# Kernel optimization log

Hardware: AMD Instinct MI355X
Metric: run time of the kernel (lower is better)

The kernel has to match this reference:

```python
import jax, jax.numpy as jnp
import numpy as np
from jax import lax

HEADS = 4
DIM_HEAD = 64


def setup_inputs() -> dict:
    key = jax.random.key(0)
    k1, k2, k3 = jax.random.split(key, 3)
    B, C, H, W = 4, 256, 64, 64
    x = jax.random.normal(k1, (B, C, H, W), dtype=jnp.float32)
    # depthwise 3x3 conv weight, groups=C -> OIHW with O=C, I=1
    w_dw = jax.random.normal(k2, (C, 1, 3, 3), dtype=jnp.float32) * 0.1
    # pointwise 1x1 conv weight C -> 3C (stored as [out, in])
    w_pw = jax.random.normal(k3, (3 * C, C), dtype=jnp.float32) * 0.05
    return {"x": x, "w_dw": w_dw, "w_pw": w_pw}


def reference(x, w_dw, w_pw):
    B, C, H, W = x.shape
    S = H * W
    scale = DIM_HEAD ** -0.5
    # depthwise separable conv QKV projection (no bias)
    dw = lax.conv_general_dilated(
        x, w_dw, window_strides=(1, 1), padding=((1, 1), (1, 1)),
        feature_group_count=C, dimension_numbers=("NCHW", "OIHW", "NCHW"))
    qkv = jnp.einsum("bchw,oc->bohw", dw, w_pw)  # [B, 3C, H, W]
    q, k, v = jnp.split(qkv, 3, axis=1)

    def to_heads(t):
        # b (h d) ih iw -> b h (ih iw) d
        t = t.reshape(B, HEADS, DIM_HEAD, S)
        return jnp.transpose(t, (0, 1, 3, 2))  # [B, h, S, d]

    q, k, v = to_heads(q), to_heads(k), to_heads(v)
    dots = jnp.einsum("bhsd,bhtd->bhst", q, k) * scale  # [B, h, S, S]
    attn = jax.nn.softmax(dots, axis=-1)
    out = jnp.einsum("bhst,bhtd->bhsd", attn, v)  # [B, h, S, d]
    # b h (ih iw) d -> b (h d) ih iw
    out = jnp.transpose(out, (0, 1, 3, 2)).reshape(B, C, H, W)
    return out
```

## Files before the change

### kernel.cpp

```cpp
#include <hip/hip_runtime.h>


typedef __attribute__((ext_vector_type(8))) __bf16 bf16x8;
typedef __attribute__((ext_vector_type(4))) float f32x4;
typedef __attribute__((ext_vector_type(16))) float f32x16;
typedef __attribute__((ext_vector_type(8))) unsigned short ushort8;
typedef __attribute__((ext_vector_type(4))) unsigned int uint4v;

#define OFF_DW 0ull
#define OFF_WB 8388608ull
#define OFF_Q  8781824ull
#define OFF_K  17170432ull
#define OFF_V  25559040ull

__device__ __forceinline__ unsigned short f2bf(float x) {
  unsigned u = __builtin_bit_cast(unsigned, x);
  u += 0x7fffu + ((u >> 16) & 1u);
  return (unsigned short)(u >> 16);
}

__device__ __forceinline__ void gld16(const void* g, void* l) {
  __builtin_amdgcn_global_load_lds((const __attribute__((address_space(1))) void*)g,
                                   (__attribute__((address_space(3))) void*)l, 16, 0, 0);
}

__device__ __forceinline__ unsigned cvtpk(float lo, float hi) {
  unsigned r;
  asm("v_cvt_pk_bf16_f32 %0, %1, %2" : "=v"(r) : "v"(lo), "v"(hi));
  return r;
}

__global__ __launch_bounds__(256) void k_wcvt(const float* __restrict__ wpw,
                                              unsigned short* __restrict__ wbf) {
  int idx = blockIdx.x * 256 + threadIdx.x;
  int o = idx >> 8;
  float v = wpw[idx];
  if (o < 256) v *= 0.18033688011112042f;
  wbf[idx] = f2bf(v);
}

__global__ __launch_bounds__(256) void k_dw(const float* __restrict__ x,
                                            const float* __restrict__ wdw,
                                            unsigned short* __restrict__ dwt) {
  __shared__ float tile[64 * 65];
  const int t = threadIdx.x;
  const int h = blockIdx.x;
  const int c0 = blockIdx.y * 64;
  const int b = blockIdx.z;
  const int w = t & 63;
  const int wq = t >> 6;
#pragma unroll
  for (int i = 0; i < 16; ++i) {
    int cl = wq * 16 + i;
    int c = c0 + cl;
    const float* wd = wdw + c * 9;
    const float* xb = x + ((size_t)(b * 256 + c) * 64) * 64;
    float acc = 0.f;
#pragma unroll
    for (int ky = 0; ky < 3; ++ky) {
      int hh = h + ky - 1;
      if ((unsigned)hh < 64u) {
        const float* row = xb + hh * 64;
#pragma unroll
        for (int kx = 0; kx < 3; ++kx) {
          int ww = w + kx - 1;
          if ((unsigned)ww < 64u) acc += row[ww] * wd[ky * 3 + kx];
        }
      }
    }
    tile[w * 65 + cl] = acc;
  }
  __syncthreads();
  int sl = t >> 2, cch = (t & 3) * 16;
  ushort8 p0, p1;
#pragma unroll
  for (int j = 0; j < 8; ++j) p0[j] = f2bf(tile[sl * 65 + cch + j]);
#pragma unroll
  for (int j = 0; j < 8; ++j) p1[j] = f2bf(tile[sl * 65 + cch + 8 + j]);
  unsigned short* dst = dwt + ((size_t)(b * 4096 + h * 64 + sl)) * 256 + c0 + cch;
  *(ushort8*)dst = p0;
  *(ushort8*)(dst + 8) = p1;
}

__global__ __launch_bounds__(512) void k_pw(const unsigned short* __restrict__ dwt,
                                            const unsigned short* __restrict__ wbf,
                                            unsigned short* __restrict__ q,
                                            unsigned short* __restrict__ k,
                                            unsigned short* __restrict__ v) {
  __shared__ __align__(16) unsigned char smem[114944];
  const int t = threadIdx.x;
  const int lane = t & 63, wv = t >> 6;
  const int s0 = blockIdx.x * 64;
  const int b = blockIdx.y;
  const int vb = ((lane >> 5) << 9) + (((lane & 31) ^ (lane >> 5)) << 4);
  const char* dsrc = (const char*)dwt + ((size_t)(b * 4096 + s0)) * 512;
#pragma unroll
  for (int i = 0; i < 4; ++i) {
    int I = wv * 4 + i;
    int u = ((2 * i) & 7) << 4;
    gld16(dsrc + (size_t)I * 1024 + (vb ^ u), smem + 65536 + I * 1024);
    gld16((const char*)wbf + (size_t)I * 1024 + (vb ^ u), smem + I * 1024);
  }
  asm volatile("s_waitcnt vmcnt(0)" ::: "memory");
  __syncthreads();

  const int c15 = lane & 15, g = lane >> 4;
  const int wo = wv >> 1, ws = wv & 1;
  const int orow = wo * 16 + c15;

#pragma unroll 1
  for (int yy = 0; yy < 12; ++yy) {
    const unsigned char* wbuf = smem + (yy & 1) * 32768;
    if (yy < 11) {
      unsigned char* wnext = smem + ((yy + 1) & 1) * 32768;
#pragma unroll
      for (int i = 0; i < 4; ++i) {
        int I = wv * 4 + i;
        int u = ((2 * i) & 7) << 4;
        gld16((const char*)wbf + (size_t)(yy + 1) * 32768 + (size_t)I * 1024 + (vb ^ u),
              wnext + I * 1024);
      }
    }

    f32x4 acc[2] = {{0,0,0,0},{0,0,0,0}};
#pragma unroll
    for (int kc = 0; kc < 8; ++kc) {
      bf16x8 a = *(const bf16x8*)(wbuf + orow * 512 + (((kc * 4 + g) ^ (orow & 7)) << 4));
#pragma unroll
      for (int nt = 0; nt < 2; ++nt) {
        int srow = (ws * 2 + nt) * 16 + c15;
        bf16x8 bb = *(const bf16x8*)(smem + 65536 + srow * 512 + (((kc * 4 + g) ^ (srow & 7)) << 4));
        acc[nt] = __builtin_amdgcn_mfma_f32_16x16x32_bf16(a, bb, acc[nt], 0, 0, 0);
      }
    }

    const int type = yy >> 2, head = yy & 3;
    const size_t bh = (size_t)(b * 4 + head);
    if (type == 2) {
#pragma unroll
      for (int nt = 0; nt < 2; ++nt)
#pragma unroll
        for (int r = 0; r < 4; ++r) {
          int d = wo * 16 + g * 4 + r;
          int sg = s0 + (ws * 2 + nt) * 16 + c15;
          v[(bh * 64 + d) * 4096 + sg] = f2bf(acc[nt][r]);
        }
    } else {
      float* ol = (float*)(smem + 98304);
#pragma unroll
      for (int nt = 0; nt < 2; ++nt)
#pragma unroll
        for (int r = 0; r < 4; ++r)
          ol[((ws * 2 + nt) * 16 + c15) * 65 + (wo * 16 + g * 4 + r)] = acc[nt][r];
      __syncthreads();
      unsigned short* dst0 = (type == 0) ? q : k;
      int sl = t >> 3, dch = (t & 7) * 8;
      ushort8 p0;
#pragma unroll
      for (int j = 0; j < 8; ++j) p0[j] = f2bf(ol[sl * 65 + dch + j]);
      unsigned short* dst = dst0 + (bh * 4096 + s0 + sl) * 64 + dch;
      *(ushort8*)dst = p0;
    }

    asm volatile("s_waitcnt vmcnt(0)" ::: "memory");
    __syncthreads();
  }
}

__global__ __launch_bounds__(512) void k_attn(const unsigned short* __restrict__ qg,
                                              const unsigned short* __restrict__ kg,
                                              const unsigned short* __restrict__ vg,
                                              float* __restrict__ out) {
  __shared__ __align__(16) unsigned char smem[98304];
  const int t = threadIdx.x;
  const int lane = t & 63, wv = t >> 6;
  const int l31 = lane & 31, hi = lane >> 5;

  const int blk = blockIdx.x;
  const int xcd = blk & 7, idx = blk >> 3;
  const int bh = xcd * 2 + (idx & 1);
  const int s0 = (idx >> 1) * 256;

  const char* qsrc = (const char*)qg + (size_t)bh * 524288 + (size_t)s0 * 128;
  const char* ksrc = (const char*)kg + (size_t)bh * 524288;
  const char* vsrc = (const char*)vg + (size_t)bh * 524288;
  const int vQK = ((lane >> 3) << 7) + (((lane & 7) ^ (lane >> 3)) << 4);
  const int vV  = ((lane >> 3) << 13) + (((lane & 7) ^ (lane >> 3)) << 4);
  int kpoff[2];
  {
#pragma unroll
    for (int i = 0; i < 2; ++i) {
      int I = (wv & 3) * 2 + i;
      int srb = I * 8 + (lane >> 3);
      if (((srb >> 2) + 1) & 2) srb ^= 12;
      kpoff[i] = srb * 128 + (((lane & 7) ^ (lane >> 3)) << 4);
    }
  }

#pragma unroll
  for (int i = 0; i < 4; ++i) {
    int I = wv * 4 + i;
    gld16(qsrc + (size_t)I * 1024 + vQK, smem + I * 1024);
  }
#pragma unroll
  for (int tt = 0; tt < 2; ++tt) {
    unsigned char* tb = smem + 32768 + tt * 16384;
    if (wv < 4) {
#pragma unroll
      for (int i = 0; i < 2; ++i) {
        int I = wv * 2 + i;
        gld16(ksrc + (size_t)tt * 8192 + kpoff[i], tb + I * 1024);
      }
    } else {
#pragma unroll
      for (int i = 0; i < 2; ++i) {
        int I = (wv - 4) * 2 + i;
        gld16(vsrc + (size_t)tt * 128 + (size_t)I * 65536 + vV, tb + 8192 + I * 1024);
      }
    }
  }
  asm volatile("s_waitcnt vmcnt(2)" ::: "memory");
  __builtin_amdgcn_s_barrier();
  asm volatile("" ::: "memory");

  bf16x8 qf[4];
  {
    int row = wv * 32 + l31;
#pragma unroll
    for (int ks = 0; ks < 4; ++ks)
      qf[ks] = *(const bf16x8*)(smem + row * 128 + (((ks * 2 + hi) ^ (row & 7)) << 4));
  }

  f32x16 O0, O1, lacc;
#pragma unroll
  for (int r = 0; r < 16; ++r) { O0[r] = 0.f; O1[r] = 0.f; lacc[r] = 0.f; }

  uint4v onesu;
  onesu[0] = onesu[1] = onesu[2] = onesu[3] = 0x3F803F80u;
  const bf16x8 onesb = __builtin_bit_cast(bf16x8, onesu);

#pragma unroll 4
  for (int it = 0; it < 64; ++it) {
    const unsigned char* kb = smem + 32768 + (it & 3) * 16384;
    const unsigned char* vbuf = kb + 8192;
    if (it < 62) {
      unsigned char* nb = smem + 32768 + ((it + 2) & 3) * 16384;
      if (wv < 4) {
#pragma unroll
        for (int i = 0; i < 2; ++i) {
          int I = wv * 2 + i;
          gld16(ksrc + (size_t)(it + 2) * 8192 + kpoff[i], nb + I * 1024);
        }
      } else {
#pragma unroll
        for (int i = 0; i < 2; ++i) {
          int I = (wv - 4) * 2 + i;
          gld16(vsrc + (size_t)(it + 2) * 128 + (size_t)I * 65536 + vV, nb + 8192 + I * 1024);
        }
      }
    }

    f32x16 sc0, sc1;
#pragma unroll
    for (int r = 0; r < 16; ++r) { sc0[r] = 0.f; sc1[r] = 0.f; }
    __builtin_amdgcn_s_setprio(1);
#pragma unroll
    for (int ks = 0; ks < 4; ++ks) {
      int sw = ((ks * 2 + hi) ^ (l31 & 7)) << 4;
      bf16x8 kf0 = *(const bf16x8*)(kb + l31 * 128 + sw);
      sc0 = __builtin_amdgcn_mfma_f32_32x32x16_bf16(kf0, qf[ks], sc0, 0, 0, 0);
      bf16x8 kf1 = *(const bf16x8*)(kb + (32 + l31) * 128 + sw);
      sc1 = __builtin_amdgcn_mfma_f32_32x32x16_bf16(kf1, qf[ks], sc1, 0, 0, 0);
    }
    __builtin_amdgcn_s_setprio(0);

#pragma unroll
    for (int r = 0; r < 16; ++r) {
      sc0[r] = __builtin_amdgcn_exp2f(sc0[r]);
      sc1[r] = __builtin_amdgcn_exp2f(sc1[r]);
    }

    uint4v paw[4];
#pragma unroll
    for (int j = 0; j < 4; ++j) {
      paw[0][j] = cvtpk(sc0[2 * j],     sc0[2 * j + 1]);
      paw[1][j] = cvtpk(sc0[8 + 2 * j], sc0[8 + 2 * j + 1]);
      paw[2][j] = cvtpk(sc1[2 * j],     sc1[2 * j + 1]);
      paw[3][j] = cvtpk(sc1[8 + 2 * j], sc1[8 + 2 * j + 1]);
    }

    __builtin_amdgcn_s_setprio(1);
#pragma unroll
    for (int ks = 0; ks < 4; ++ks) {
      bf16x8 pa = __builtin_bit_cast(bf16x8, paw[ks]);
      lacc = __builtin_amdgcn_mfma_f32_32x32x16_bf16(pa, onesb, lacc, 0, 0, 0);
      int sw = ((ks * 2 + hi) ^ (l31 & 7)) << 4;
      bf16x8 v0 = *(const bf16x8*)(vbuf + l31 * 128 + sw);
      O0 = __builtin_amdgcn_mfma_f32_32x32x16_bf16(pa, v0, O0, 0, 0, 0);
      bf16x8 v1 = *(const bf16x8*)(vbuf + (32 + l31) * 128 + sw);
      O1 = __builtin_amdgcn_mfma_f32_32x32x16_bf16(pa, v1, O1, 0, 0, 0);
    }
    __builtin_amdgcn_s_setprio(0);

    if (it < 62) {
      asm volatile("s_waitcnt vmcnt(2)" ::: "memory");
    } else {
      asm volatile("s_waitcnt vmcnt(0)" ::: "memory");
    }
    __builtin_amdgcn_s_barrier();
    asm volatile("" ::: "memory");
  }

  float rn[16];
#pragma unroll
  for (int r = 0; r < 16; ++r) rn[r] = 1.0f / lacc[r];
  float* ep = (float*)(smem + wv * 4608);
  const size_t outbase = (size_t)bh * 262144 + (size_t)(s0 + wv * 32);
#pragma unroll
  for (int dt = 0; dt < 2; ++dt) {
    const f32x16& O = dt ? O1 : O0;
#pragma unroll
    for (int g4 = 0; g4 < 4; ++g4) {
      f32x4 w;
      w[0] = O[4 * g4 + 0] * rn[4 * g4 + 0];
      w[1] = O[4 * g4 + 1] * rn[4 * g4 + 1];
      w[2] = O[4 * g4 + 2] * rn[4 * g4 + 2];
      w[3] = O[4 * g4 + 3] * rn[4 * g4 + 3];
      *(f32x4*)(ep + l31 * 36 + g4 * 8 + hi * 4) = w;
    }
#pragma unroll
    for (int j = 0; j < 4; ++j) {
      int idx2 = j * 64 + lane;
      int d = idx2 >> 3, s4c = idx2 & 7;
      f32x4 vv = *(const f32x4*)(ep + d * 36 + s4c * 4);
      *(f32x4*)(out + outbase + (size_t)(dt * 32 + d) * 4096 + s4c * 4) = vv;
    }
  }
}

extern "C" void kernel_launch(void* const* d_in, const int* in_sizes, int n_in,
                              void* d_out, int out_size, void* d_ws, size_t ws_size,
                              hipStream_t stream) {
  const float* x = (const float*)d_in[0];
  const float* wdw = (const float*)d_in[1];
  const float* wpw = (const float*)d_in[2];
  float* out = (float*)d_out;
  char* ws = (char*)d_ws;
  unsigned short* dwt = (unsigned short*)(ws + OFF_DW);
  unsigned short* wbf = (unsigned short*)(ws + OFF_WB);
  unsigned short* q = (unsigned short*)(ws + OFF_Q);
  unsigned short* k = (unsigned short*)(ws + OFF_K);
  unsigned short* v = (unsigned short*)(ws + OFF_V);

  k_wcvt<<<dim3(768), dim3(256), 0, stream>>>(wpw, wbf);
  k_dw<<<dim3(64, 4, 4), dim3(256), 0, stream>>>(x, wdw, dwt);
  k_pw<<<dim3(64, 4), dim3(512), 0, stream>>>(dwt, wbf, q, k, v);
  k_attn<<<dim3(256), dim3(512), 0, stream>>>(q, k, v, out);
}
```

Baseline: 139.7 us.

## Fuse depthwise conv into pointwise projection kernel and pair attention tiles per barrier

```diff
diff --git a/kernel.cpp b/kernel.cpp
--- a/kernel.cpp
+++ b/kernel.cpp
@@ -7,11 +7,10 @@
 typedef __attribute__((ext_vector_type(8))) unsigned short ushort8;
 typedef __attribute__((ext_vector_type(4))) unsigned int uint4v;
 
-#define OFF_DW 0ull
-#define OFF_WB 8388608ull
-#define OFF_Q  8781824ull
-#define OFF_K  17170432ull
-#define OFF_V  25559040ull
+#define OFF_WB 0ull
+#define OFF_Q  524288ull
+#define OFF_K  8912896ull
+#define OFF_V  17301504ull
 
 __device__ __forceinline__ unsigned short f2bf(float x) {
   unsigned u = __builtin_bit_cast(unsigned, x);
@@ -39,67 +38,55 @@
   wbf[idx] = f2bf(v);
 }
 
-__global__ __launch_bounds__(256) void k_dw(const float* __restrict__ x,
-                                            const float* __restrict__ wdw,
-                                            unsigned short* __restrict__ dwt) {
-  __shared__ float tile[64 * 65];
-  const int t = threadIdx.x;
-  const int h = blockIdx.x;
-  const int c0 = blockIdx.y * 64;
-  const int b = blockIdx.z;
-  const int w = t & 63;
-  const int wq = t >> 6;
-#pragma unroll
-  for (int i = 0; i < 16; ++i) {
-    int cl = wq * 16 + i;
-    int c = c0 + cl;
-    const float* wd = wdw + c * 9;
-    const float* xb = x + ((size_t)(b * 256 + c) * 64) * 64;
-    float acc = 0.f;
-#pragma unroll
-    for (int ky = 0; ky < 3; ++ky) {
-      int hh = h + ky - 1;
-      if ((unsigned)hh < 64u) {
-        const float* row = xb + hh * 64;
-#pragma unroll
-        for (int kx = 0; kx < 3; ++kx) {
-          int ww = w + kx - 1;
-          if ((unsigned)ww < 64u) acc += row[ww] * wd[ky * 3 + kx];
-        }
-      }
-    }
-    tile[w * 65 + cl] = acc;
-  }
-  __syncthreads();
-  int sl = t >> 2, cch = (t & 3) * 16;
-  ushort8 p0, p1;
-#pragma unroll
-  for (int j = 0; j < 8; ++j) p0[j] = f2bf(tile[sl * 65 + cch + j]);
-#pragma unroll
-  for (int j = 0; j < 8; ++j) p1[j] = f2bf(tile[sl * 65 + cch + 8 + j]);
-  unsigned short* dst = dwt + ((size_t)(b * 4096 + h * 64 + sl)) * 256 + c0 + cch;
-  *(ushort8*)dst = p0;
-  *(ushort8*)(dst + 8) = p1;
-}
-
-__global__ __launch_bounds__(512) void k_pw(const unsigned short* __restrict__ dwt,
-                                            const unsigned short* __restrict__ wbf,
-                                            unsigned short* __restrict__ q,
-                                            unsigned short* __restrict__ k,
-                                            unsigned short* __restrict__ v) {
+__global__ __launch_bounds__(512) void k_fused(const float* __restrict__ x,
+                                               const float* __restrict__ wdw,
+                                               const unsigned short* __restrict__ wbf,
+                                               unsigned short* __restrict__ q,
+                                               unsigned short* __restrict__ k,
+                                               unsigned short* __restrict__ v) {
   __shared__ __align__(16) unsigned char smem[114944];
   const int t = threadIdx.x;
   const int lane = t & 63, wv = t >> 6;
-  const int s0 = blockIdx.x * 64;
+  const int hh = blockIdx.x;
   const int b = blockIdx.y;
+  const int s0 = hh * 64;
   const int vb = ((lane >> 5) << 9) + (((lane & 31) ^ (lane >> 5)) << 4);
-  const char* dsrc = (const char*)dwt + ((size_t)(b * 4096 + s0)) * 512;
+
 #pragma unroll
   for (int i = 0; i < 4; ++i) {
     int I = wv * 4 + i;
     int u = ((2 * i) & 7) << 4;
-    gld16(dsrc + (size_t)I * 1024 + (vb ^ u), smem + 65536 + I * 1024);
     gld16((const char*)wbf + (size_t)I * 1024 + (vb ^ u), smem + I * 1024);
+  }
+
+  {
+    const int w = t >> 3, j = t & 7;
+#pragma unroll
+    for (int jj = 0; jj < 4; ++jj) {
+      int ch = jj * 8 + j;
+      ushort8 pk;
+#pragma unroll
+      for (int ci = 0; ci < 8; ++ci) {
+        int c = ch * 8 + ci;
+        const float* wd = wdw + c * 9;
+        const float* xb = x + ((size_t)(b * 256 + c) << 12);
+        float acc = 0.f;
+#pragma unroll
+        for (int ky = 0; ky < 3; ++ky) {
+          int h2 = hh + ky - 1;
+          if ((unsigned)h2 < 64u) {
+            const float* row = xb + h2 * 64;
+#pragma unroll
+            for (int kx = 0; kx < 3; ++kx) {
+              int ww = w + kx - 1;
+              if ((unsigned)ww < 64u) acc += row[ww] * wd[ky * 3 + kx];
+            }
+          }
+        }
+        pk[ci] = f2bf(acc);
+      }
+      *(ushort8*)(smem + 65536 + w * 512 + ((ch ^ (w & 7)) << 4)) = pk;
+    }
   }
   asm volatile("s_waitcnt vmcnt(0)" ::: "memory");
   __syncthreads();
@@ -197,29 +184,31 @@
     }
   }
 
+  auto stage = [&](int tt, int bufid) {
+    unsigned char* tb = smem + 32768 + bufid * 16384;
+    if (wv < 4) {
+#pragma unroll
+      for (int i = 0; i < 2; ++i) {
+        int I = wv * 2 + i;
+        gld16(ksrc + (size_t)tt * 8192 + kpoff[i], tb + I * 1024);
+      }
+    } else {
+#pragma unroll
+      for (int i = 0; i < 2; ++i) {
+        int I = (wv - 4) * 2 + i;
+        gld16(vsrc + (size_t)tt * 128 + (size_t)I * 65536 + vV, tb + 8192 + I * 1024);
+      }
+    }
+  };
+
 #pragma unroll
   for (int i = 0; i < 4; ++i) {
     int I = wv * 4 + i;
     gld16(qsrc + (size_t)I * 1024 + vQK, smem + I * 1024);
   }
-#pragma unroll
-  for (int tt = 0; tt < 2; ++tt) {
-    unsigned char* tb = smem + 32768 + tt * 16384;
-    if (wv < 4) {
-#pragma unroll
-      for (int i = 0; i < 2; ++i) {
-        int I = wv * 2 + i;
-        gld16(ksrc + (size_t)tt * 8192 + kpoff[i], tb + I * 1024);
-      }
-    } else {
-#pragma unroll
-      for (int i = 0; i < 2; ++i) {
-        int I = (wv - 4) * 2 + i;
-        gld16(vsrc + (size_t)tt * 128 + (size_t)I * 65536 + vV, tb + 8192 + I * 1024);
-      }
-    }
-  }
-  asm volatile("s_waitcnt vmcnt(2)" ::: "memory");
+  stage(0, 0);
+  stage(1, 1);
+  asm volatile("s_waitcnt vmcnt(0)" ::: "memory");
   __builtin_amdgcn_s_barrier();
   asm volatile("" ::: "memory");
 
@@ -239,27 +228,8 @@
   onesu[0] = onesu[1] = onesu[2] = onesu[3] = 0x3F803F80u;
   const bf16x8 onesb = __builtin_bit_cast(bf16x8, onesu);
 
-#pragma unroll 4
-  for (int it = 0; it < 64; ++it) {
-    const unsigned char* kb = smem + 32768 + (it & 3) * 16384;
+  auto tile_body = [&](const unsigned char* kb) {
     const unsigned char* vbuf = kb + 8192;
-    if (it < 62) {
-      unsigned char* nb = smem + 32768 + ((it + 2) & 3) * 16384;
-      if (wv < 4) {
-#pragma unroll
-        for (int i = 0; i < 2; ++i) {
-          int I = wv * 2 + i;
-          gld16(ksrc + (size_t)(it + 2) * 8192 + kpoff[i], nb + I * 1024);
-        }
-      } else {
-#pragma unroll
-        for (int i = 0; i < 2; ++i) {
-          int I = (wv - 4) * 2 + i;
-          gld16(vsrc + (size_t)(it + 2) * 128 + (size_t)I * 65536 + vV, nb + 8192 + I * 1024);
-        }
-      }
-    }
-
     f32x16 sc0, sc1;
 #pragma unroll
     for (int r = 0; r < 16; ++r) { sc0[r] = 0.f; sc1[r] = 0.f; }
@@ -301,12 +271,17 @@
       O1 = __builtin_amdgcn_mfma_f32_32x32x16_bf16(pa, v1, O1, 0, 0, 0);
     }
     __builtin_amdgcn_s_setprio(0);
-
-    if (it < 62) {
-      asm volatile("s_waitcnt vmcnt(2)" ::: "memory");
-    } else {
-      asm volatile("s_waitcnt vmcnt(0)" ::: "memory");
-    }
+  };
+
+#pragma unroll 2
+  for (int p = 0; p < 32; ++p) {
+    if (p < 31) {
+      stage(2 * p + 2, (2 * p + 2) & 3);
+      stage(2 * p + 3, (2 * p + 3) & 3);
+    }
+    tile_body(smem + 32768 + ((2 * p) & 3) * 16384);
+    tile_body(smem + 32768 + ((2 * p + 1) & 3) * 16384);
+    asm volatile("s_waitcnt vmcnt(0)" ::: "memory");
     __builtin_amdgcn_s_barrier();
     asm volatile("" ::: "memory");
   }
@@ -346,14 +321,12 @@
   const float* wpw = (const float*)d_in[2];
   float* out = (float*)d_out;
   char* ws = (char*)d_ws;
-  unsigned short* dwt = (unsigned short*)(ws + OFF_DW);
   unsigned short* wbf = (unsigned short*)(ws + OFF_WB);
   unsigned short* q = (unsigned short*)(ws + OFF_Q);
   unsigned short* k = (unsigned short*)(ws + OFF_K);
   unsigned short* v = (unsigned short*)(ws + OFF_V);
 
   k_wcvt<<<dim3(768), dim3(256), 0, stream>>>(wpw, wbf);
-  k_dw<<<dim3(64, 4, 4), dim3(256), 0, stream>>>(x, wdw, dwt);
-  k_pw<<<dim3(64, 4), dim3(512), 0, stream>>>(dwt, wbf, q, k, v);
+  k_fused<<<dim3(64, 4), dim3(512), 0, stream>>>(x, wdw, wbf, q, k, v);
   k_attn<<<dim3(256), dim3(512), 0, stream>>>(q, k, v, out);
 }
```

Result: slower. 171.1 us (+22.5%).
